# Kernel optimization log

Hardware: AMD Instinct MI355X
Metric: run time of the kernel (lower is better)

Reference implementation:

```python
import jax, jax.numpy as jnp
import numpy as np
import math

HID = 128      # hidden_dim == d_inner (expand=1)
NSTATE = 8     # d_state
K = 4          # scan directions
RANK = math.ceil(HID / 16)  # dt_rank = 8
B, H, W = 4, 64, 64


def _ln(x, g, b, eps=1e-5):
    m = jnp.mean(x, -1, keepdims=True)
    v = jnp.mean((x - m) ** 2, -1, keepdims=True)
    return (x - m) * jax.lax.rsqrt(v + eps) * g + b


def _ss2d(x, in_w, conv_w, conv_b, xproj_w, dt_w, dt_b, A_logs, Ds, ln_g, ln_b, out_w):
    # x: [B,H,W,C] -> VMamba SS2D with d_inner=C, 4-direction selective scan
    Bn, Hh, Ww, C = x.shape
    D, L = C, Hh * Ww
    N = A_logs.shape[-1]
    R = dt_w.shape[-1]
    xz = x @ in_w.T                      # [B,H,W,2D]
    xc, z = jnp.split(xz, 2, axis=-1)
    xc = xc.transpose(0, 3, 1, 2)        # [B,D,H,W]
    xc = jax.lax.conv_general_dilated(xc, conv_w, (1, 1), 'SAME', feature_group_count=D)
    xc = jax.nn.silu(xc + conv_b[None, :, None, None])
    x_hw = xc.reshape(Bn, D, L)
    x_wh = xc.transpose(0, 1, 3, 2).reshape(Bn, D, L)
    xs = jnp.stack([x_hw, x_wh, x_hw[..., ::-1], x_wh[..., ::-1]], 1)  # [B,K,D,L]
    x_dbl = jnp.einsum('bkdl,kcd->bkcl', xs, xproj_w)
    dts, Bs, Cs = x_dbl[:, :, :R], x_dbl[:, :, R:R + N], x_dbl[:, :, R + N:]
    dt = jax.nn.softplus(jnp.einsum('bkrl,kdr->bkdl', dts, dt_w) + dt_b[None, :, :, None])
    A = -jnp.exp(A_logs.reshape(K, D, N))  # [K,D,N]

    def step(h, inp):
        x_t, dt_t, B_t, C_t = inp          # [B,K,D],[B,K,D],[B,K,N],[B,K,N]
        h = h * jnp.exp(dt_t[..., None] * A) + dt_t[..., None] * B_t[:, :, None, :] * x_t[..., None]
        return h, jnp.einsum('bkdn,bkn->bkd', h, C_t)

    h0 = jnp.zeros((Bn, K, D, N), x.dtype)
    _, ys = jax.lax.scan(step, h0, (xs.transpose(3, 0, 1, 2), dt.transpose(3, 0, 1, 2),
                                    Bs.transpose(3, 0, 1, 2), Cs.transpose(3, 0, 1, 2)))
    out_y = ys.transpose(1, 2, 3, 0) + Ds.reshape(K, D)[None, :, :, None] * xs  # [B,K,D,L]
    wh_y = out_y[:, 3, :, ::-1].reshape(Bn, D, Ww, Hh).transpose(0, 1, 3, 2).reshape(Bn, D, L)
    invwh_y = out_y[:, 1].reshape(Bn, D, Ww, Hh).transpose(0, 1, 3, 2).reshape(Bn, D, L)
    y = out_y[:, 0] + out_y[:, 2, :, ::-1] + wh_y + invwh_y
    y = _ln(y.transpose(0, 2, 1).reshape(Bn, Hh, Ww, D), ln_g, ln_b)
    return (y * jax.nn.silu(z)) @ out_w.T


def _enhance(x, g, b, w, bias):
    return jax.nn.gelu(_ln(x, g, b) @ w.T + bias, approximate=False)


def setup_inputs() -> dict:
    key = jax.random.key(0)
    ks = jax.random.split(key, 12)
    f = lambda k, s, sc=0.02: jax.random.normal(k, s, jnp.float32) * sc
    return dict(
        sar_feat=jax.random.normal(ks[0], (B, H, W, HID), jnp.float32),
        opt_feat=jax.random.normal(ks[1], (B, H, W, HID), jnp.float32),
        ss_in_w=f(ks[2], (2, 2 * HID, HID)),
        ss_conv_w=f(ks[3], (2, HID, 1, 3, 3), 0.1),
        ss_conv_b=f(ks[4], (2, HID)),
        ss_xproj_w=f(ks[5], (2, K, RANK + 2 * NSTATE, HID)),
        ss_dt_w=f(ks[6], (2, K, HID, RANK), 0.1),
        ss_dt_b=f(ks[7], (2, K, HID), 0.1),
        ss_Alogs=jnp.tile(jnp.log(jnp.arange(1, NSTATE + 1, dtype=jnp.float32)), (2, K * HID, 1)),
        ss_Ds=jnp.ones((2, K * HID), jnp.float32),
        ss_ln_g=jnp.ones((2, HID), jnp.float32),
        ss_ln_b=jnp.zeros((2, HID), jnp.float32),
        ss_out_w=f(ks[8], (2, HID, HID)),
        enh_ln_g=jnp.ones((2, HID), jnp.float32),
        enh_ln_b=jnp.zeros((2, HID), jnp.float32),
        enh_w=f(ks[9], (2, HID, HID)),
        enh_b=jnp.zeros((2, HID), jnp.float32),
    )


def reference(sar_feat, opt_feat, ss_in_w, ss_conv_w, ss_conv_b, ss_xproj_w, ss_dt_w,
              ss_dt_b, ss_Alogs, ss_Ds, ss_ln_g, ss_ln_b, ss_out_w,
              enh_ln_g, enh_ln_b, enh_w, enh_b):
    # cat([opt,sar],-1)[...,:C] == opt ; cat([sar,opt],-1)[...,:C] == sar (faithful identity slice)
    # index 0 = cross_ss2d_s2o (input opt), index 1 = cross_ss2d_o2s (input sar)
    xin = jnp.stack([opt_feat, sar_feat])
    guided = jax.vmap(_ss2d)(xin, ss_in_w, ss_conv_w, ss_conv_b, ss_xproj_w, ss_dt_w,
                             ss_dt_b, ss_Alogs, ss_Ds, ss_ln_g, ss_ln_b, ss_out_w)
    # enhance params: index 0 = enhance_sar (on sar_guided=guided[1]), index 1 = enhance_opt (on opt_guided=guided[0])
    enh_in = jnp.stack([guided[1], guided[0]])
    enhanced = jax.vmap(_enhance)(enh_in, enh_ln_g, enh_ln_b, enh_w, enh_b)
    return (sar_feat + enhanced[0], opt_feat + enhanced[1])
```

## Files before the change

kernel.cpp:

```cpp
#include <hip/hip_runtime.h>
#include <hip/hip_bf16.h>
#include <math.h>

#define DEV __device__ __forceinline__

static constexpr int LL = 4096;
static constexpr int DD = 128;
static constexpr int SEG = 128;
static constexpr float LOG2E = 1.4426950408889634f;
static constexpr float LN2 = 0.6931471805599453f;

DEV float silu_(float x) { return x / (1.f + __expf(-x)); }
DEV float erf_(float x) {
  const float ax = fabsf(x);
  const float t = 1.f / fmaf(0.3275911f, ax, 1.f);
  float p = fmaf(1.061405429f, t, -1.453152027f);
  p = fmaf(p, t, 1.421413741f);
  p = fmaf(p, t, -0.284496736f);
  p = fmaf(p, t, 0.254829592f);
  p = p * t;
  const float r = 1.f - p * __expf(-ax * ax);
  return x < 0.f ? -r : r;
}
DEV float gelu_(float x) { return 0.5f * x * (1.f + erf_(x * 0.7071067811865475f)); }
DEV float sp_(float x) {
  const float t = __builtin_amdgcn_exp2f(-fabsf(x) * LOG2E);
  return fmaxf(x, 0.f) + LN2 * __builtin_amdgcn_logf(1.f + t);
}

template <int CTRL>
DEV float dpp_add_(float x) {
  int y = __builtin_amdgcn_update_dpp(0, __float_as_int(x), CTRL, 0xF, 0xF, true);
  return x + __int_as_float(y);
}

DEV void seg_base_step(int k, int s, int& base, int& step) {
  if (k == 0)      { base = s * 64;        step = 1;   }
  else if (k == 1) { base = s;             step = 64;  }
  else if (k == 2) { base = 4095 - s * 64; step = -1;  }
  else             { base = 4095 - s;      step = -64; }
}

__global__ __launch_bounds__(256) void k_inproj(
    const float* __restrict__ sar, const float* __restrict__ opt,
    const float* __restrict__ in_w, float* __restrict__ xz) {
  const int lt = blockIdx.x, ct = blockIdx.y, mb = blockIdx.z;
  const int m = mb >> 2;
  const float* __restrict__ x = (m == 0 ? opt : sar) + (size_t)(mb & 3) * (LL * DD);
  const float* __restrict__ W = in_w + (size_t)m * 256 * DD;
  __shared__ float sA[64][68];
  __shared__ float sW[64][68];
  const int tid = threadIdx.x;
  const int tc = tid & 15, tl = tid >> 4;
  float acc[4][4] = {};
  for (int db = 0; db < 2; ++db) {
    __syncthreads();
    for (int idx = tid; idx < 64 * 16; idx += 256) {
      const int r = idx >> 4, d4 = (idx & 15) << 2;
      *(float4*)&sA[r][d4] = *(const float4*)&x[(size_t)(lt * 64 + r) * DD + db * 64 + d4];
      *(float4*)&sW[r][d4] = *(const float4*)&W[(size_t)(ct * 64 + r) * DD + db * 64 + d4];
    }
    __syncthreads();
#pragma unroll 4
    for (int d = 0; d < 64; d += 4) {
      float4 a[4], w[4];
#pragma unroll
      for (int q = 0; q < 4; ++q) a[q] = *(const float4*)&sA[tl * 4 + q][d];
#pragma unroll
      for (int j = 0; j < 4; ++j) w[j] = *(const float4*)&sW[tc + 16 * j][d];
#pragma unroll
      for (int j = 0; j < 4; ++j)
#pragma unroll
        for (int q = 0; q < 4; ++q)
          acc[j][q] += a[q].x * w[j].x + a[q].y * w[j].y + a[q].z * w[j].z + a[q].w * w[j].w;
    }
  }
  float* __restrict__ dst = xz + ((size_t)mb * 256 + ct * 64) * LL + lt * 64;
#pragma unroll
  for (int j = 0; j < 4; ++j) {
    float4 v = make_float4(acc[j][0], acc[j][1], acc[j][2], acc[j][3]);
    *(float4*)&dst[(size_t)(tc + 16 * j) * LL + tl * 4] = v;
  }
}

__global__ __launch_bounds__(256) void k_conv(
    const float* __restrict__ xz, const float* __restrict__ conv_w,
    const float* __restrict__ conv_b, float* __restrict__ xc) {
  const int ht = blockIdx.x, dg = blockIdx.y, mb = blockIdx.z;
  const int m = mb >> 2;
  __shared__ float sIn[8][18][66];
  __shared__ float sOut[1024][8];
  const float* __restrict__ src = xz + ((size_t)mb * 256 + dg * 8) * LL;
  const int tid = threadIdx.x;
  for (int idx = tid; idx < 8 * 18 * 66; idx += 256) {
    const int dd = idx / (18 * 66);
    const int rem = idx - dd * (18 * 66);
    const int hh = rem / 66, ww = rem - hh * 66;
    const int h = ht * 16 + hh - 1, w = ww - 1;
    float v = 0.f;
    if (h >= 0 && h < 64 && w >= 0 && w < 64) v = src[(size_t)dd * LL + h * 64 + w];
    sIn[dd][hh][ww] = v;
  }
  __syncthreads();
  const int dd = tid & 7, wv = tid >> 3;
  const int dch = dg * 8 + dd;
  float wk[9];
#pragma unroll
  for (int t = 0; t < 9; ++t) wk[t] = conv_w[((size_t)m * DD + dch) * 9 + t];
  const float bias = conv_b[m * DD + dch];
  for (int hh = 0; hh < 16; ++hh) {
#pragma unroll
    for (int wh = 0; wh < 2; ++wh) {
      const int w = wv + wh * 32;
      float s = bias;
#pragma unroll
      for (int kh = 0; kh < 3; ++kh)
#pragma unroll
        for (int kw = 0; kw < 3; ++kw)
          s = fmaf(sIn[dd][hh + kh][w + kw], wk[kh * 3 + kw], s);
      sOut[hh * 64 + w][dd] = silu_(s);
    }
  }
  __syncthreads();
  float* __restrict__ dst = xc + (size_t)mb * LL * DD + dg * 8;
#pragma unroll
  for (int r = 0; r < 4; ++r) {
    const int pos = tid + r * 256;
    const int l = ht * 1024 + pos;
    *(float4*)&dst[(size_t)l * DD + 0] = *(const float4*)&sOut[pos][0];
    *(float4*)&dst[(size_t)l * DD + 4] = *(const float4*)&sOut[pos][4];
  }
}

__global__ __launch_bounds__(256) void k_xproj(
    const float* __restrict__ xc, const float* __restrict__ xproj_w,
    float* __restrict__ xdbl) {
  const int lt = blockIdx.x, k = blockIdx.y, mb = blockIdx.z;
  const int m = mb >> 2, mbk = mb * 4 + k;
  __shared__ float sX[64][132];
  __shared__ float sW[24][132];
  const int tid = threadIdx.x;
  const float* __restrict__ src = xc + (size_t)mb * LL * DD;
  int base, step;
  seg_base_step(k, lt, base, step);
  for (int idx = tid; idx < 64 * 32; idx += 256) {
    const int l = idx >> 5, d4 = (idx & 31) << 2;
    *(float4*)&sX[l][d4] = *(const float4*)&src[(size_t)(base + l * step) * DD + d4];
  }
  const float* __restrict__ Wsrc = xproj_w + ((size_t)m * 4 + k) * 24 * DD;
  for (int idx = tid; idx < 24 * 32; idx += 256) {
    const int r = idx >> 5, d4 = (idx & 31) << 2;
    *(float4*)&sW[r][d4] = *(const float4*)&Wsrc[(size_t)r * DD + d4];
  }
  __syncthreads();
  const int l = tid >> 2, cg = tid & 3;
  float acc[6] = {};
#pragma unroll 8
  for (int d = 0; d < 128; d += 4) {
    const float4 xv = *(const float4*)&sX[l][d];
#pragma unroll
    for (int j = 0; j < 6; ++j) {
      const float4 wv = *(const float4*)&sW[cg * 6 + j][d];
      acc[j] += xv.x * wv.x + xv.y * wv.y + xv.z * wv.z + xv.w * wv.w;
    }
  }
  float* __restrict__ dst = xdbl + ((size_t)mbk * LL + lt * 64 + l) * 24 + cg * 6;
#pragma unroll
  for (int j = 0; j < 6; ++j) dst[j] = acc[j];
}


DEV void load_aln2(const float* __restrict__ Alogs, int m, int k, int d,
                   float* __restrict__ aln2, bool& fastp) {
  const float4 a0 = *(const float4*)&Alogs[((size_t)m * 512 + k * DD + d) * 8];
  const float4 a1 = *(const float4*)&Alogs[((size_t)m * 512 + k * DD + d) * 8 + 4];
  aln2[0] = -__expf(a0.x) * LOG2E; aln2[1] = -__expf(a0.y) * LOG2E;
  aln2[2] = -__expf(a0.z) * LOG2E; aln2[3] = -__expf(a0.w) * LOG2E;
  aln2[4] = -__expf(a1.x) * LOG2E; aln2[5] = -__expf(a1.y) * LOG2E;
  aln2[6] = -__expf(a1.z) * LOG2E; aln2[7] = -__expf(a1.w) * LOG2E;
  fastp = true;
#pragma unroll
  for (int n = 1; n < 8; ++n)
    fastp = fastp && (fabsf(aln2[n] - (float)(n + 1) * aln2[0]) <=
                      1e-4f * fabsf(aln2[n]) + 1e-12f);
}

DEV void load_w8(const float* __restrict__ dt_w, int mbk, int d,
                 float* __restrict__ wreg) {
  const float4 w0 = *(const float4*)&dt_w[((size_t)mbk * DD + d) * 8];
  const float4 w1 = *(const float4*)&dt_w[((size_t)mbk * DD + d) * 8 + 4];
  wreg[0] = w0.x; wreg[1] = w0.y; wreg[2] = w0.z; wreg[3] = w0.w;
  wreg[4] = w1.x; wreg[5] = w1.y; wreg[6] = w1.z; wreg[7] = w1.w;
}

template <bool FAST>
DEV void qpow_(float dt, const float* __restrict__ aln2, float* __restrict__ q) {
  if constexpr (FAST) {
    q[0] = __builtin_amdgcn_exp2f(dt * aln2[0]);
    q[1] = q[0] * q[0]; q[2] = q[1] * q[0]; q[3] = q[1] * q[1];
    q[4] = q[3] * q[0]; q[5] = q[3] * q[1]; q[6] = q[3] * q[2]; q[7] = q[3] * q[3];
  } else {
#pragma unroll
    for (int n = 0; n < 8; ++n) q[n] = __builtin_amdgcn_exp2f(dt * aln2[n]);
  }
}

DEV float dt_of_(const float* __restrict__ slds, int j,
                 const float* __restrict__ w, float bw) {
  const float4 t0 = *(const float4*)&slds[j * 24 + 0];
  const float4 t1 = *(const float4*)&slds[j * 24 + 4];
  float s = bw;
  s = fmaf(t0.x, w[0], s); s = fmaf(t0.y, w[1], s);
  s = fmaf(t0.z, w[2], s); s = fmaf(t0.w, w[3], s);
  s = fmaf(t1.x, w[4], s); s = fmaf(t1.y, w[5], s);
  s = fmaf(t1.z, w[6], s); s = fmaf(t1.w, w[7], s);
  return sp_(s);
}

template <bool FAST>
DEV void hstep_(const float* __restrict__ slds, int j, float dt, float x,
                const float* __restrict__ aln2, float* __restrict__ h) {
  const float u = dt * x;
  float q[8];
  qpow_<FAST>(dt, aln2, q);
  const float4 b0 = *(const float4*)&slds[j * 24 + 8];
  const float4 b1 = *(const float4*)&slds[j * 24 + 12];
  h[0] = fmaf(h[0], q[0], u * b0.x);
  h[1] = fmaf(h[1], q[1], u * b0.y);
  h[2] = fmaf(h[2], q[2], u * b0.z);
  h[3] = fmaf(h[3], q[3], u * b0.w);
  h[4] = fmaf(h[4], q[4], u * b1.x);
  h[5] = fmaf(h[5], q[5], u * b1.y);
  h[6] = fmaf(h[6], q[6], u * b1.z);
  h[7] = fmaf(h[7], q[7], u * b1.w);
}

template <bool FAST>
DEV float ystep_(const float* __restrict__ slds, int j, float dt, float x,
                 const float* __restrict__ aln2, float dsv,
                 float* __restrict__ h) {
  const float u = dt * x;
  float q[8];
  qpow_<FAST>(dt, aln2, q);
  const float4 b0 = *(const float4*)&slds[j * 24 + 8];
  const float4 b1 = *(const float4*)&slds[j * 24 + 12];
  const float4 c0 = *(const float4*)&slds[j * 24 + 16];
  const float4 c1 = *(const float4*)&slds[j * 24 + 20];
  float y = dsv * x;
  h[0] = fmaf(h[0], q[0], u * b0.x); y = fmaf(h[0], c0.x, y);
  h[1] = fmaf(h[1], q[1], u * b0.y); y = fmaf(h[1], c0.y, y);
  h[2] = fmaf(h[2], q[2], u * b0.z); y = fmaf(h[2], c0.z, y);
  h[3] = fmaf(h[3], q[3], u * b0.w); y = fmaf(h[3], c0.w, y);
  h[4] = fmaf(h[4], q[4], u * b1.x); y = fmaf(h[4], c1.x, y);
  h[5] = fmaf(h[5], q[5], u * b1.y); y = fmaf(h[5], c1.y, y);
  h[6] = fmaf(h[6], q[6], u * b1.z); y = fmaf(h[6], c1.z, y);
  h[7] = fmaf(h[7], q[7], u * b1.w); y = fmaf(h[7], c1.w, y);
  return y;
}

template <bool FAST>
DEV void loop1d_(const float* __restrict__ sldsA, const float* __restrict__ sldsB,
                 const float* __restrict__ sx, int d,
                 const float* __restrict__ aln2A, const float* __restrict__ aln2B,
                 const float* __restrict__ wA, const float* __restrict__ wB,
                 float bwA, float bwB, float* __restrict__ hA,
                 float* __restrict__ hB, float& dtsA, float& dtsB) {
#pragma unroll 8
  for (int j = 0; j < 32; ++j) {
    const float xA = sx[j * 128 + d];
    const float xB = sx[(31 - j) * 128 + d];
    const float dtA = dt_of_(sldsA, j, wA, bwA);
    const float dtB = dt_of_(sldsB, j, wB, bwB);
    dtsA += dtA; dtsB += dtB;
    hstep_<FAST>(sldsA, j, dtA, xA, aln2A, hA);
    hstep_<FAST>(sldsB, j, dtB, xB, aln2B, hB);
  }
}

__global__ __launch_bounds__(128) void k_scan1(
    const float* __restrict__ xc, const float* __restrict__ xdbl,
    const float* __restrict__ dt_w, const float* __restrict__ dt_b,
    const float* __restrict__ Alogs, float* __restrict__ hend,
    float* __restrict__ Pseg) {
  const int s = blockIdx.x, p = blockIdx.y, mb = blockIdx.z;
  const int m = mb >> 2;
  const int kA = p, kB = p + 2;
  const int sA = s, sB = 127 - s;
  const int mbkA = mb * 4 + kA, mbkB = mb * 4 + kB;
  const int d = threadIdx.x;
  __shared__ float sldsA[32 * 24], sldsB[32 * 24];
  __shared__ float sx[32 * 128];

  const float4* tA = (const float4*)(xdbl + ((size_t)mbkA * LL + sA * 32) * 24);
  const float4* tB = (const float4*)(xdbl + ((size_t)mbkB * LL + sB * 32) * 24);
  ((float4*)sldsA)[d] = tA[d];
  if (d < 64) ((float4*)sldsA)[128 + d] = tA[128 + d];
  ((float4*)sldsB)[d] = tB[d];
  if (d < 64) ((float4*)sldsB)[128 + d] = tB[128 + d];

  const int base0 = (p == 0) ? s * 32 : ((s & 1) * 32) * 64 + (s >> 1);
  const int stepPos = (p == 0) ? 1 : 64;
  const float* __restrict__ xsrc = xc + (size_t)mb * LL * DD;
#pragma unroll
  for (int t = 0; t < 8; ++t) {
    const int idx = d + t * 128;
    const int r = idx >> 5, c4 = (idx & 31) << 2;
    ((float4*)sx)[idx] = *(const float4*)&xsrc[(size_t)(base0 + r * stepPos) * DD + c4];
  }

  float aln2A[8], aln2B[8]; bool fA, fB;
  load_aln2(Alogs, m, kA, d, aln2A, fA);
  load_aln2(Alogs, m, kB, d, aln2B, fB);
  float wA[8], wB[8];
  load_w8(dt_w, mbkA, d, wA);
  load_w8(dt_w, mbkB, d, wB);
  const float bwA = dt_b[(size_t)mbkA * DD + d];
  const float bwB = dt_b[(size_t)mbkB * DD + d];
  __syncthreads();

  float hA[8] = {0, 0, 0, 0, 0, 0, 0, 0};
  float hB[8] = {0, 0, 0, 0, 0, 0, 0, 0};
  float dtsA = 0.f, dtsB = 0.f;
  if (fA && fB)
    loop1d_<true>(sldsA, sldsB, sx, d, aln2A, aln2B, wA, wB, bwA, bwB, hA, hB, dtsA, dtsB);
  else
    loop1d_<false>(sldsA, sldsB, sx, d, aln2A, aln2B, wA, wB, bwA, bwB, hA, hB, dtsA, dtsB);

  {
    float* __restrict__ he = hend + (((size_t)mbkA * SEG + sA) << 10) + d * 8;
    float* __restrict__ pe = Pseg + (((size_t)mbkA * SEG + sA) << 10) + d * 8;
    *(float4*)&he[0] = make_float4(hA[0], hA[1], hA[2], hA[3]);
    *(float4*)&he[4] = make_float4(hA[4], hA[5], hA[6], hA[7]);
    *(float4*)&pe[0] = make_float4(
        __builtin_amdgcn_exp2f(aln2A[0] * dtsA), __builtin_amdgcn_exp2f(aln2A[1] * dtsA),
        __builtin_amdgcn_exp2f(aln2A[2] * dtsA), __builtin_amdgcn_exp2f(aln2A[3] * dtsA));
    *(float4*)&pe[4] = make_float4(
        __builtin_amdgcn_exp2f(aln2A[4] * dtsA), __builtin_amdgcn_exp2f(aln2A[5] * dtsA),
        __builtin_amdgcn_exp2f(aln2A[6] * dtsA), __builtin_amdgcn_exp2f(aln2A[7] * dtsA));
  }
  {
    float* __restrict__ he = hend + (((size_t)mbkB * SEG + sB) << 10) + d * 8;
    float* __restrict__ pe = Pseg + (((size_t)mbkB * SEG + sB) << 10) + d * 8;
    *(float4*)&he[0] = make_float4(hB[0], hB[1], hB[2], hB[3]);
    *(float4*)&he[4] = make_float4(hB[4], hB[5], hB[6], hB[7]);
    *(float4*)&pe[0] = make_float4(
        __builtin_amdgcn_exp2f(aln2B[0] * dtsB), __builtin_amdgcn_exp2f(aln2B[1] * dtsB),
        __builtin_amdgcn_exp2f(aln2B[2] * dtsB), __builtin_amdgcn_exp2f(aln2B[3] * dtsB));
    *(float4*)&pe[4] = make_float4(
        __builtin_amdgcn_exp2f(aln2B[4] * dtsB), __builtin_amdgcn_exp2f(aln2B[5] * dtsB),
        __builtin_amdgcn_exp2f(aln2B[6] * dtsB), __builtin_amdgcn_exp2f(aln2B[7] * dtsB));
  }
}

__global__ __launch_bounds__(256) void k_scan2(
    const float* __restrict__ hend, const float* __restrict__ Pseg,
    float* __restrict__ hin) {
  const int gid = blockIdx.x * 256 + threadIdx.x;
  const int mbk = gid >> 10, dn = gid & 1023;
  const float* __restrict__ P = Pseg + ((size_t)mbk * SEG << 10) + dn;
  const float* __restrict__ E = hend + ((size_t)mbk * SEG << 10) + dn;
  float* __restrict__ O = hin + ((size_t)mbk * SEG << 10) + dn;
  float h = 0.f;
#pragma unroll
  for (int s = 0; s < SEG; ++s) {
    O[(size_t)s << 10] = h;
    if (s < SEG - 1) h = fmaf(P[(size_t)s << 10], h, E[(size_t)s << 10]);
  }
}

template <bool FAST>
DEV void loop3d_(const float* __restrict__ sldsA, const float* __restrict__ sldsB,
                 const float* __restrict__ sx, int d,
                 const float* __restrict__ aln2A, const float* __restrict__ aln2B,
                 const float* __restrict__ wA, const float* __restrict__ wB,
                 float bwA, float bwB, float dsvA, float dsvB,
                 float* __restrict__ hA, float* __restrict__ hB,
                 float* __restrict__ yA, float* __restrict__ yB,
                 ptrdiff_t sstep) {
#pragma unroll 8
  for (int j = 0; j < 32; ++j) {
    const float xA = sx[j * 128 + d];
    const float xB = sx[(31 - j) * 128 + d];
    const float dtA = dt_of_(sldsA, j, wA, bwA);
    const float dtB = dt_of_(sldsB, j, wB, bwB);
    const float vA = ystep_<FAST>(sldsA, j, dtA, xA, aln2A, dsvA, hA);
    const float vB = ystep_<FAST>(sldsB, j, dtB, xB, aln2B, dsvB, hB);
    yA[(ptrdiff_t)j * sstep] = vA;
    yB[(ptrdiff_t)(31 - j) * sstep] = vB;
  }
}

__global__ __launch_bounds__(128) void k_scan3(
    const float* __restrict__ xc, const float* __restrict__ xdbl,
    const float* __restrict__ dt_w, const float* __restrict__ dt_b,
    const float* __restrict__ Alogs, const float* __restrict__ Ds,
    const float* __restrict__ hin, float* __restrict__ y0,
    float* __restrict__ y1, float* __restrict__ y2, float* __restrict__ y3) {
  const int s = blockIdx.x, p = blockIdx.y, mb = blockIdx.z;
  const int m = mb >> 2;
  const int kA = p, kB = p + 2;
  const int sA = s, sB = 127 - s;
  const int mbkA = mb * 4 + kA, mbkB = mb * 4 + kB;
  const int d = threadIdx.x;
  __shared__ float sldsA[32 * 24], sldsB[32 * 24];
  __shared__ float sx[32 * 128];

  const float4* tA = (const float4*)(xdbl + ((size_t)mbkA * LL + sA * 32) * 24);
  const float4* tB = (const float4*)(xdbl + ((size_t)mbkB * LL + sB * 32) * 24);
  ((float4*)sldsA)[d] = tA[d];
  if (d < 64) ((float4*)sldsA)[128 + d] = tA[128 + d];
  ((float4*)sldsB)[d] = tB[d];
  if (d < 64) ((float4*)sldsB)[128 + d] = tB[128 + d];

  const int base0 = (p == 0) ? s * 32 : ((s & 1) * 32) * 64 + (s >> 1);
  const int stepPos = (p == 0) ? 1 : 64;
  const float* __restrict__ xsrc = xc + (size_t)mb * LL * DD;
#pragma unroll
  for (int t = 0; t < 8; ++t) {
    const int idx = d + t * 128;
    const int r = idx >> 5, c4 = (idx & 31) << 2;
    ((float4*)sx)[idx] = *(const float4*)&xsrc[(size_t)(base0 + r * stepPos) * DD + c4];
  }

  float aln2A[8], aln2B[8]; bool fA, fB;
  load_aln2(Alogs, m, kA, d, aln2A, fA);
  load_aln2(Alogs, m, kB, d, aln2B, fB);
  float wA[8], wB[8];
  load_w8(dt_w, mbkA, d, wA);
  load_w8(dt_w, mbkB, d, wB);
  const float bwA = dt_b[(size_t)mbkA * DD + d];
  const float bwB = dt_b[(size_t)mbkB * DD + d];
  const float dsvA = Ds[(size_t)m * 512 + kA * DD + d];
  const float dsvB = Ds[(size_t)m * 512 + kB * DD + d];

  float hA[8], hB[8];
  {
    const float* hp = hin + (((size_t)mbkA * SEG + sA) << 10) + d * 8;
    const float4 h0 = *(const float4*)&hp[0];
    const float4 h1 = *(const float4*)&hp[4];
    hA[0] = h0.x; hA[1] = h0.y; hA[2] = h0.z; hA[3] = h0.w;
    hA[4] = h1.x; hA[5] = h1.y; hA[6] = h1.z; hA[7] = h1.w;
  }
  {
    const float* hp = hin + (((size_t)mbkB * SEG + sB) << 10) + d * 8;
    const float4 h0 = *(const float4*)&hp[0];
    const float4 h1 = *(const float4*)&hp[4];
    hB[0] = h0.x; hB[1] = h0.y; hB[2] = h0.z; hB[3] = h0.w;
    hB[4] = h1.x; hB[5] = h1.y; hB[6] = h1.z; hB[7] = h1.w;
  }

  const size_t off0 = (size_t)mb * LL * DD + (size_t)base0 * DD + d;
  float* __restrict__ yA = (p == 0 ? y0 : y1) + off0;
  float* __restrict__ yB = (p == 0 ? y2 : y3) + off0;
  const ptrdiff_t sstep = (ptrdiff_t)stepPos * DD;
  __syncthreads();

  if (fA && fB)
    loop3d_<true>(sldsA, sldsB, sx, d, aln2A, aln2B, wA, wB, bwA, bwB,
                  dsvA, dsvB, hA, hB, yA, yB, sstep);
  else
    loop3d_<false>(sldsA, sldsB, sx, d, aln2A, aln2B, wA, wB, bwA, bwB,
                   dsvA, dsvB, hA, hB, yA, yB, sstep);
}

__global__ __launch_bounds__(256) void k_outproj(
    const float* __restrict__ y0, const float* __restrict__ y1,
    const float* __restrict__ y2, const float* __restrict__ y3,
    const float* __restrict__ xz, const float* __restrict__ ln_g,
    const float* __restrict__ ln_b, const float* __restrict__ out_w,
    float* __restrict__ guided) {
  const int lt = blockIdx.x, mb = blockIdx.y;
  const int m = mb >> 2;
  __shared__ float sv[32][132];
  __shared__ float sW[64][68];
  __shared__ float smr[32][2];
  __shared__ float sg[128], sb[128];
  const int tid = threadIdx.x;
  const size_t yoff = ((size_t)mb * LL + lt * 32) * DD;
  const float4* p0 = (const float4*)(y0 + yoff);
  const float4* p1 = (const float4*)(y1 + yoff);
  const float4* p2 = (const float4*)(y2 + yoff);
  const float4* p3 = (const float4*)(y3 + yoff);
  float4 ya[4], yb[4], yc4[4], yd4[4];
#pragma unroll
  for (int t = 0; t < 4; ++t) {
    ya[t] = p0[tid + t * 256]; yb[t] = p1[tid + t * 256];
    yc4[t] = p2[tid + t * 256]; yd4[t] = p3[tid + t * 256];
  }
  const int zc = tid >> 1, zh = tid & 1;
  const float4* zsrc = (const float4*)(xz + ((size_t)mb * 256 + 128 + zc) * LL + lt * 32 + zh * 16);
  float4 zv[4];
#pragma unroll
  for (int t = 0; t < 4; ++t) zv[t] = zsrc[t];
  const float* __restrict__ Wp = out_w + (size_t)m * DD * DD;
  float4 wpre[4];
#pragma unroll
  for (int t = 0; t < 4; ++t) {
    const int idx = tid + t * 256;
    wpre[t] = *(const float4*)&Wp[(size_t)(idx >> 4) * DD + ((idx & 15) << 2)];
  }
  if (tid < 128) { sg[tid] = ln_g[m * DD + tid]; sb[tid] = ln_b[m * DD + tid]; }
#pragma unroll
  for (int t = 0; t < 4; ++t) {
    const int idx = tid + t * 256;
    float4 v;
    v.x = (ya[t].x + yb[t].x) + (yc4[t].x + yd4[t].x);
    v.y = (ya[t].y + yb[t].y) + (yc4[t].y + yd4[t].y);
    v.z = (ya[t].z + yb[t].z) + (yc4[t].z + yd4[t].z);
    v.w = (ya[t].w + yb[t].w) + (yc4[t].w + yd4[t].w);
    *(float4*)&sv[idx >> 5][(idx & 31) << 2] = v;
  }
  __syncthreads();
  {
    const int l = tid >> 3, q = tid & 7;
    float s = 0.f, s2 = 0.f;
#pragma unroll
    for (int d0 = 0; d0 < 16; d0 += 4) {
      const float4 v = *(const float4*)&sv[l][q * 16 + d0];
      s += v.x + v.y + v.z + v.w;
      s2 += v.x * v.x + v.y * v.y + v.z * v.z + v.w * v.w;
    }
    s = dpp_add_<0xB1>(s); s = dpp_add_<0x4E>(s); s = dpp_add_<0x141>(s);
    s2 = dpp_add_<0xB1>(s2); s2 = dpp_add_<0x4E>(s2); s2 = dpp_add_<0x141>(s2);
    if (q == 0) {
      const float mean = s * (1.f / 128.f);
      smr[l][0] = mean;
      smr[l][1] = rsqrtf(fmaf(s2, 1.f / 128.f, -mean * mean) + 1e-5f);
    }
  }
  __syncthreads();
  {
    const float g = sg[zc], bb = sb[zc];
    const float* zf = (const float*)zv;
#pragma unroll
    for (int i2 = 0; i2 < 16; ++i2) {
      const int l = zh * 16 + i2;
      const float v = fmaf((sv[l][zc] - smr[l][0]) * smr[l][1], g, bb);
      sv[l][zc] = v * silu_(zf[i2]);
    }
  }
  const int tc = tid & 15, tl = tid >> 4;
  float* __restrict__ dst = guided + ((size_t)mb * LL + lt * 32) * DD;
#pragma unroll
  for (int jb = 0; jb < 2; ++jb) {
    float acc[4][2] = {};
#pragma unroll
    for (int db = 0; db < 2; ++db) {
      __syncthreads();
#pragma unroll
      for (int t = 0; t < 4; ++t) {
        const int idx = tid + t * 256;
        *(float4*)&sW[idx >> 4][(idx & 15) << 2] = wpre[t];
      }
      const int ph = jb * 2 + db + 1;
      if (ph < 4) {
        const int jb2 = ph >> 1, db2 = ph & 1;
#pragma unroll
        for (int t = 0; t < 4; ++t) {
          const int idx = tid + t * 256;
          wpre[t] = *(const float4*)&Wp[(size_t)(jb2 * 64 + (idx >> 4)) * DD + db2 * 64 + ((idx & 15) << 2)];
        }
      }
      __syncthreads();
#pragma unroll 4
      for (int d0 = 0; d0 < 64; d0 += 4) {
        float4 av[2], wv[4];
#pragma unroll
        for (int q = 0; q < 2; ++q) av[q] = *(const float4*)&sv[tl * 2 + q][db * 64 + d0];
#pragma unroll
        for (int j = 0; j < 4; ++j) wv[j] = *(const float4*)&sW[tc + 16 * j][d0];
#pragma unroll
        for (int j = 0; j < 4; ++j)
#pragma unroll
          for (int q = 0; q < 2; ++q)
            acc[j][q] += av[q].x * wv[j].x + av[q].y * wv[j].y + av[q].z * wv[j].z + av[q].w * wv[j].w;
      }
    }
#pragma unroll
    for (int j = 0; j < 4; ++j)
#pragma unroll
      for (int q = 0; q < 2; ++q)
        dst[(size_t)(tl * 2 + q) * DD + jb * 64 + tc + 16 * j] = acc[j][q];
  }
}

__global__ __launch_bounds__(256) void k_enhance(
    const float* __restrict__ guided, const float* __restrict__ eg,
    const float* __restrict__ ebv, const float* __restrict__ ew,
    const float* __restrict__ ebias, const float* __restrict__ sar,
    const float* __restrict__ opt, float* __restrict__ outp) {
  const int lt = blockIdx.x, ib = blockIdx.y;
  const int i = ib >> 2, b = ib & 3;
  __shared__ float sv[32][132];
  __shared__ float sW[64][68];
  __shared__ float smr[32][2];
  __shared__ float sg[128], sb2[128], sbias[128];
  const int tid = threadIdx.x;
  const float4* gsrc =
      (const float4*)(guided + (((size_t)(1 - i) * 4 + b) * LL + lt * 32) * DD);
  float4 gv[4];
#pragma unroll
  for (int t = 0; t < 4; ++t) gv[t] = gsrc[tid + t * 256];
  const float* __restrict__ Wp = ew + (size_t)i * DD * DD;
  float4 wpre[4];
#pragma unroll
  for (int t = 0; t < 4; ++t) {
    const int idx = tid + t * 256;
    wpre[t] = *(const float4*)&Wp[(size_t)(idx >> 4) * DD + ((idx & 15) << 2)];
  }
  if (tid < 128) {
    sg[tid] = eg[i * DD + tid];
    sb2[tid] = ebv[i * DD + tid];
    sbias[tid] = ebias[i * DD + tid];
  }
#pragma unroll
  for (int t = 0; t < 4; ++t) {
    const int idx = tid + t * 256;
    *(float4*)&sv[idx >> 5][(idx & 31) << 2] = gv[t];
  }
  __syncthreads();
  {
    const int l = tid >> 3, q = tid & 7;
    float s = 0.f, s2 = 0.f;
#pragma unroll
    for (int d0 = 0; d0 < 16; d0 += 4) {
      const float4 v = *(const float4*)&sv[l][q * 16 + d0];
      s += v.x + v.y + v.z + v.w;
      s2 += v.x * v.x + v.y * v.y + v.z * v.z + v.w * v.w;
    }
    s = dpp_add_<0xB1>(s); s = dpp_add_<0x4E>(s); s = dpp_add_<0x141>(s);
    s2 = dpp_add_<0xB1>(s2); s2 = dpp_add_<0x4E>(s2); s2 = dpp_add_<0x141>(s2);
    if (q == 0) {
      const float mean = s * (1.f / 128.f);
      smr[l][0] = mean;
      smr[l][1] = rsqrtf(fmaf(s2, 1.f / 128.f, -mean * mean) + 1e-5f);
    }
  }
  __syncthreads();
  {
    const int c = tid >> 1, half = tid & 1;
    const float g = sg[c], bb = sb2[c];
#pragma unroll
    for (int i2 = 0; i2 < 16; ++i2) {
      const int l = half * 16 + i2;
      sv[l][c] = fmaf((sv[l][c] - smr[l][0]) * smr[l][1], g, bb);
    }
  }
  const int tc = tid & 15, tl = tid >> 4;
  const float* __restrict__ resid = (i == 0 ? sar : opt) + ((size_t)b * LL + lt * 32) * DD;
  float* __restrict__ dst = outp + (size_t)i * (4 * LL * DD) + ((size_t)b * LL + lt * 32) * DD;
  float rv[16];
#pragma unroll
  for (int jb = 0; jb < 2; ++jb)
#pragma unroll
    for (int j = 0; j < 4; ++j)
#pragma unroll
      for (int q = 0; q < 2; ++q)
        rv[jb * 8 + j * 2 + q] = resid[(size_t)(tl * 2 + q) * DD + jb * 64 + tc + 16 * j];
  float accA[4][2] = {}, accB[4][2] = {};
#pragma unroll
  for (int jb = 0; jb < 2; ++jb) {
#pragma unroll
    for (int db = 0; db < 2; ++db) {
      __syncthreads();
#pragma unroll
      for (int t = 0; t < 4; ++t) {
        const int idx = tid + t * 256;
        *(float4*)&sW[idx >> 4][(idx & 15) << 2] = wpre[t];
      }
      const int ph = jb * 2 + db + 1;
      if (ph < 4) {
        const int jb2 = ph >> 1, db2 = ph & 1;
#pragma unroll
        for (int t = 0; t < 4; ++t) {
          const int idx = tid + t * 256;
          wpre[t] = *(const float4*)&Wp[(size_t)(jb2 * 64 + (idx >> 4)) * DD + db2 * 64 + ((idx & 15) << 2)];
        }
      }
      __syncthreads();
      float (*acc)[2] = (jb == 0) ? accA : accB;
#pragma unroll 4
      for (int d0 = 0; d0 < 64; d0 += 4) {
        float4 av[2], wv[4];
#pragma unroll
        for (int q = 0; q < 2; ++q) av[q] = *(const float4*)&sv[tl * 2 + q][db * 64 + d0];
#pragma unroll
        for (int j = 0; j < 4; ++j) wv[j] = *(const float4*)&sW[tc + 16 * j][d0];
#pragma unroll
        for (int j = 0; j < 4; ++j)
#pragma unroll
          for (int q = 0; q < 2; ++q)
            acc[j][q] += av[q].x * wv[j].x + av[q].y * wv[j].y + av[q].z * wv[j].z + av[q].w * wv[j].w;
      }
    }
  }
#pragma unroll
  for (int jb = 0; jb < 2; ++jb)
#pragma unroll
    for (int j = 0; j < 4; ++j)
#pragma unroll
      for (int q = 0; q < 2; ++q) {
        const int col = jb * 64 + tc + 16 * j;
        const float u = ((jb == 0) ? accA[j][q] : accB[j][q]) + sbias[col];
        dst[(size_t)(tl * 2 + q) * DD + col] = rv[jb * 8 + j * 2 + q] + gelu_(u);
      }
}

extern "C" void kernel_launch(void* const* d_in, const int* in_sizes, int n_in,
                              void* d_out, int out_size, void* d_ws, size_t ws_size,
                              hipStream_t stream) {
  (void)in_sizes; (void)n_in; (void)out_size; (void)ws_size;
  const float* sar    = (const float*)d_in[0];
  const float* opt    = (const float*)d_in[1];
  const float* in_w   = (const float*)d_in[2];
  const float* conv_w = (const float*)d_in[3];
  const float* conv_b = (const float*)d_in[4];
  const float* xproj_w= (const float*)d_in[5];
  const float* dt_w   = (const float*)d_in[6];
  const float* dt_b   = (const float*)d_in[7];
  const float* Alogs  = (const float*)d_in[8];
  const float* Ds     = (const float*)d_in[9];
  const float* ln_g   = (const float*)d_in[10];
  const float* ln_b   = (const float*)d_in[11];
  const float* out_w  = (const float*)d_in[12];
  const float* eg     = (const float*)d_in[13];
  const float* eb     = (const float*)d_in[14];
  const float* ew     = (const float*)d_in[15];
  const float* ebias  = (const float*)d_in[16];

  float* ws     = (float*)d_ws;
  float* xz     = ws;
  float* xc     = xz + 8388608;
  float* xdbl   = xc + 4194304;
  float* y0b    = xdbl + 3145728;
  float* y1b    = y0b + 4194304;
  float* y2b    = y1b + 4194304;
  float* y3b    = y2b + 4194304;
  float* guided = y3b + 4194304;
  float* hend   = guided + 4194304;
  float* Pseg   = hend + 4194304;
  float* hin    = Pseg + 4194304;
  float* outf   = (float*)d_out;

  k_inproj <<<dim3(64, 4, 8), 256, 0, stream>>>(sar, opt, in_w, xz);
  k_conv   <<<dim3(4, 16, 8), 256, 0, stream>>>(xz, conv_w, conv_b, xc);
  k_xproj  <<<dim3(64, 4, 8), 256, 0, stream>>>(xc, xproj_w, xdbl);
  k_scan1  <<<dim3(128, 2, 8), 128, 0, stream>>>(xc, xdbl, dt_w, dt_b, Alogs, hend, Pseg);
  k_scan2  <<<dim3(128), 256, 0, stream>>>(hend, Pseg, hin);
  k_scan3  <<<dim3(128, 2, 8), 128, 0, stream>>>(xc, xdbl, dt_w, dt_b, Alogs, Ds, hin,
                                                 y0b, y1b, y2b, y3b);
  k_outproj<<<dim3(128, 8), 256, 0, stream>>>(y0b, y1b, y2b, y3b, xz, ln_g, ln_b, out_w, guided);
  k_enhance<<<dim3(128, 8), 256, 0, stream>>>(guided, eg, eb, ew, ebias, sar, opt, outf);
}
```

Baseline: 265.4 us.

## Merge forward/reverse scan outputs in-register, read xdbl directly, batch scan2 loads

In k_scan3 the forward and reversed direction chains are now run one after the other per thread. The forward results are kept in a 32-entry register array and added to the reverse chain's outputs before writing. This halves the y buffers from four to two and cuts k_outproj's reads to match. Both scan kernels drop their shared-memory staging of xdbl and read it straight from global memory through cached, thread-uniform loads. k_scan2 now batches its P/E loads 16 at a time to expose memory parallelism. The cost is higher register pressure, and the A and B chains no longer interleave for ILP.

```diff
diff --git a/kernel.cpp b/kernel.cpp
--- a/kernel.cpp
+++ b/kernel.cpp
@@ -205,10 +205,10 @@
   }
 }
 
-DEV float dt_of_(const float* __restrict__ slds, int j,
+DEV float dt_of_(const float* __restrict__ t24,
                  const float* __restrict__ w, float bw) {
-  const float4 t0 = *(const float4*)&slds[j * 24 + 0];
-  const float4 t1 = *(const float4*)&slds[j * 24 + 4];
+  const float4 t0 = *(const float4*)&t24[0];
+  const float4 t1 = *(const float4*)&t24[4];
   float s = bw;
   s = fmaf(t0.x, w[0], s); s = fmaf(t0.y, w[1], s);
   s = fmaf(t0.z, w[2], s); s = fmaf(t0.w, w[3], s);
@@ -218,13 +218,13 @@
 }
 
 template <bool FAST>
-DEV void hstep_(const float* __restrict__ slds, int j, float dt, float x,
+DEV void hstep_(const float* __restrict__ t24, float dt, float x,
                 const float* __restrict__ aln2, float* __restrict__ h) {
   const float u = dt * x;
   float q[8];
   qpow_<FAST>(dt, aln2, q);
-  const float4 b0 = *(const float4*)&slds[j * 24 + 8];
-  const float4 b1 = *(const float4*)&slds[j * 24 + 12];
+  const float4 b0 = *(const float4*)&t24[8];
+  const float4 b1 = *(const float4*)&t24[12];
   h[0] = fmaf(h[0], q[0], u * b0.x);
   h[1] = fmaf(h[1], q[1], u * b0.y);
   h[2] = fmaf(h[2], q[2], u * b0.z);
@@ -236,16 +236,16 @@
 }
 
 template <bool FAST>
-DEV float ystep_(const float* __restrict__ slds, int j, float dt, float x,
+DEV float ystep_(const float* __restrict__ t24, float dt, float x,
                  const float* __restrict__ aln2, float dsv,
                  float* __restrict__ h) {
   const float u = dt * x;
   float q[8];
   qpow_<FAST>(dt, aln2, q);
-  const float4 b0 = *(const float4*)&slds[j * 24 + 8];
-  const float4 b1 = *(const float4*)&slds[j * 24 + 12];
-  const float4 c0 = *(const float4*)&slds[j * 24 + 16];
-  const float4 c1 = *(const float4*)&slds[j * 24 + 20];
+  const float4 b0 = *(const float4*)&t24[8];
+  const float4 b1 = *(const float4*)&t24[12];
+  const float4 c0 = *(const float4*)&t24[16];
+  const float4 c1 = *(const float4*)&t24[20];
   float y = dsv * x;
   h[0] = fmaf(h[0], q[0], u * b0.x); y = fmaf(h[0], c0.x, y);
   h[1] = fmaf(h[1], q[1], u * b0.y); y = fmaf(h[1], c0.y, y);
@@ -259,7 +259,7 @@
 }
 
 template <bool FAST>
-DEV void loop1d_(const float* __restrict__ sldsA, const float* __restrict__ sldsB,
+DEV void loop1d_(const float* __restrict__ tA, const float* __restrict__ tB,
                  const float* __restrict__ sx, int d,
                  const float* __restrict__ aln2A, const float* __restrict__ aln2B,
                  const float* __restrict__ wA, const float* __restrict__ wB,
@@ -269,11 +269,11 @@
   for (int j = 0; j < 32; ++j) {
     const float xA = sx[j * 128 + d];
     const float xB = sx[(31 - j) * 128 + d];
-    const float dtA = dt_of_(sldsA, j, wA, bwA);
-    const float dtB = dt_of_(sldsB, j, wB, bwB);
+    const float dtA = dt_of_(tA + j * 24, wA, bwA);
+    const float dtB = dt_of_(tB + j * 24, wB, bwB);
     dtsA += dtA; dtsB += dtB;
-    hstep_<FAST>(sldsA, j, dtA, xA, aln2A, hA);
-    hstep_<FAST>(sldsB, j, dtB, xB, aln2B, hB);
+    hstep_<FAST>(tA + j * 24, dtA, xA, aln2A, hA);
+    hstep_<FAST>(tB + j * 24, dtB, xB, aln2B, hB);
   }
 }
 
@@ -288,15 +288,10 @@
   const int sA = s, sB = 127 - s;
   const int mbkA = mb * 4 + kA, mbkB = mb * 4 + kB;
   const int d = threadIdx.x;
-  __shared__ float sldsA[32 * 24], sldsB[32 * 24];
   __shared__ float sx[32 * 128];
 
-  const float4* tA = (const float4*)(xdbl + ((size_t)mbkA * LL + sA * 32) * 24);
-  const float4* tB = (const float4*)(xdbl + ((size_t)mbkB * LL + sB * 32) * 24);
-  ((float4*)sldsA)[d] = tA[d];
-  if (d < 64) ((float4*)sldsA)[128 + d] = tA[128 + d];
-  ((float4*)sldsB)[d] = tB[d];
-  if (d < 64) ((float4*)sldsB)[128 + d] = tB[128 + d];
+  const float* __restrict__ tA = xdbl + ((size_t)mbkA * LL + sA * 32) * 24;
+  const float* __restrict__ tB = xdbl + ((size_t)mbkB * LL + sB * 32) * 24;
 
   const int base0 = (p == 0) ? s * 32 : ((s & 1) * 32) * 64 + (s >> 1);
   const int stepPos = (p == 0) ? 1 : 64;
@@ -322,9 +317,9 @@
   float hB[8] = {0, 0, 0, 0, 0, 0, 0, 0};
   float dtsA = 0.f, dtsB = 0.f;
   if (fA && fB)
-    loop1d_<true>(sldsA, sldsB, sx, d, aln2A, aln2B, wA, wB, bwA, bwB, hA, hB, dtsA, dtsB);
+    loop1d_<true>(tA, tB, sx, d, aln2A, aln2B, wA, wB, bwA, bwB, hA, hB, dtsA, dtsB);
   else
-    loop1d_<false>(sldsA, sldsB, sx, d, aln2A, aln2B, wA, wB, bwA, bwB, hA, hB, dtsA, dtsB);
+    loop1d_<false>(tA, tB, sx, d, aln2A, aln2B, wA, wB, bwA, bwB, hA, hB, dtsA, dtsB);
 
   {
     float* __restrict__ he = hend + (((size_t)mbkA * SEG + sA) << 10) + d * 8;
@@ -361,32 +356,47 @@
   const float* __restrict__ E = hend + ((size_t)mbk * SEG << 10) + dn;
   float* __restrict__ O = hin + ((size_t)mbk * SEG << 10) + dn;
   float h = 0.f;
-#pragma unroll
-  for (int s = 0; s < SEG; ++s) {
-    O[(size_t)s << 10] = h;
-    if (s < SEG - 1) h = fmaf(P[(size_t)s << 10], h, E[(size_t)s << 10]);
+  for (int c0 = 0; c0 < SEG; c0 += 16) {
+    float pv[16], ev[16];
+#pragma unroll
+    for (int t = 0; t < 16; ++t) {
+      pv[t] = P[(size_t)(c0 + t) << 10];
+      ev[t] = E[(size_t)(c0 + t) << 10];
+    }
+#pragma unroll
+    for (int t = 0; t < 16; ++t) {
+      O[(size_t)(c0 + t) << 10] = h;
+      h = fmaf(pv[t], h, ev[t]);
+    }
   }
 }
 
 template <bool FAST>
-DEV void loop3d_(const float* __restrict__ sldsA, const float* __restrict__ sldsB,
-                 const float* __restrict__ sx, int d,
-                 const float* __restrict__ aln2A, const float* __restrict__ aln2B,
-                 const float* __restrict__ wA, const float* __restrict__ wB,
-                 float bwA, float bwB, float dsvA, float dsvB,
-                 float* __restrict__ hA, float* __restrict__ hB,
-                 float* __restrict__ yA, float* __restrict__ yB,
+DEV void chainA_(const float* __restrict__ t24, const float* __restrict__ sx, int d,
+                 const float* __restrict__ aln2, const float* __restrict__ w,
+                 float bw, float dsv, float* __restrict__ h,
+                 float* __restrict__ va) {
+#pragma unroll
+  for (int j = 0; j < 32; ++j) {
+    const float x = sx[j * 128 + d];
+    const float dt = dt_of_(t24 + j * 24, w, bw);
+    va[j] = ystep_<FAST>(t24 + j * 24, dt, x, aln2, dsv, h);
+  }
+}
+
+template <bool FAST>
+DEV void chainB_(const float* __restrict__ t24, const float* __restrict__ sx, int d,
+                 const float* __restrict__ aln2, const float* __restrict__ w,
+                 float bw, float dsv, float* __restrict__ h,
+                 const float* __restrict__ va, float* __restrict__ yd,
                  ptrdiff_t sstep) {
-#pragma unroll 8
+#pragma unroll
   for (int j = 0; j < 32; ++j) {
-    const float xA = sx[j * 128 + d];
-    const float xB = sx[(31 - j) * 128 + d];
-    const float dtA = dt_of_(sldsA, j, wA, bwA);
-    const float dtB = dt_of_(sldsB, j, wB, bwB);
-    const float vA = ystep_<FAST>(sldsA, j, dtA, xA, aln2A, dsvA, hA);
-    const float vB = ystep_<FAST>(sldsB, j, dtB, xB, aln2B, dsvB, hB);
-    yA[(ptrdiff_t)j * sstep] = vA;
-    yB[(ptrdiff_t)(31 - j) * sstep] = vB;
+    const int phys = 31 - j;
+    const float x = sx[phys * 128 + d];
+    const float dt = dt_of_(t24 + j * 24, w, bw);
+    const float v = ystep_<FAST>(t24 + j * 24, dt, x, aln2, dsv, h);
+    yd[(ptrdiff_t)phys * sstep] = v + va[phys];
   }
 }
 
@@ -394,23 +404,18 @@
     const float* __restrict__ xc, const float* __restrict__ xdbl,
     const float* __restrict__ dt_w, const float* __restrict__ dt_b,
     const float* __restrict__ Alogs, const float* __restrict__ Ds,
-    const float* __restrict__ hin, float* __restrict__ y0,
-    float* __restrict__ y1, float* __restrict__ y2, float* __restrict__ y3) {
+    const float* __restrict__ hin, float* __restrict__ yrow,
+    float* __restrict__ ycol) {
   const int s = blockIdx.x, p = blockIdx.y, mb = blockIdx.z;
   const int m = mb >> 2;
   const int kA = p, kB = p + 2;
   const int sA = s, sB = 127 - s;
   const int mbkA = mb * 4 + kA, mbkB = mb * 4 + kB;
   const int d = threadIdx.x;
-  __shared__ float sldsA[32 * 24], sldsB[32 * 24];
   __shared__ float sx[32 * 128];
 
-  const float4* tA = (const float4*)(xdbl + ((size_t)mbkA * LL + sA * 32) * 24);
-  const float4* tB = (const float4*)(xdbl + ((size_t)mbkB * LL + sB * 32) * 24);
-  ((float4*)sldsA)[d] = tA[d];
-  if (d < 64) ((float4*)sldsA)[128 + d] = tA[128 + d];
-  ((float4*)sldsB)[d] = tB[d];
-  if (d < 64) ((float4*)sldsB)[128 + d] = tB[128 + d];
+  const float* __restrict__ tA = xdbl + ((size_t)mbkA * LL + sA * 32) * 24;
+  const float* __restrict__ tB = xdbl + ((size_t)mbkB * LL + sB * 32) * 24;
 
   const int base0 = (p == 0) ? s * 32 : ((s & 1) * 32) * 64 + (s >> 1);
   const int stepPos = (p == 0) ? 1 : 64;
@@ -450,22 +455,19 @@
   }
 
   const size_t off0 = (size_t)mb * LL * DD + (size_t)base0 * DD + d;
-  float* __restrict__ yA = (p == 0 ? y0 : y1) + off0;
-  float* __restrict__ yB = (p == 0 ? y2 : y3) + off0;
+  float* __restrict__ yd = (p == 0 ? yrow : ycol) + off0;
   const ptrdiff_t sstep = (ptrdiff_t)stepPos * DD;
   __syncthreads();
 
-  if (fA && fB)
-    loop3d_<true>(sldsA, sldsB, sx, d, aln2A, aln2B, wA, wB, bwA, bwB,
-                  dsvA, dsvB, hA, hB, yA, yB, sstep);
-  else
-    loop3d_<false>(sldsA, sldsB, sx, d, aln2A, aln2B, wA, wB, bwA, bwB,
-                   dsvA, dsvB, hA, hB, yA, yB, sstep);
+  float va[32];
+  if (fA) chainA_<true>(tA, sx, d, aln2A, wA, bwA, dsvA, hA, va);
+  else    chainA_<false>(tA, sx, d, aln2A, wA, bwA, dsvA, hA, va);
+  if (fB) chainB_<true>(tB, sx, d, aln2B, wB, bwB, dsvB, hB, va, yd, sstep);
+  else    chainB_<false>(tB, sx, d, aln2B, wB, bwB, dsvB, hB, va, yd, sstep);
 }
 
 __global__ __launch_bounds__(256) void k_outproj(
-    const float* __restrict__ y0, const float* __restrict__ y1,
-    const float* __restrict__ y2, const float* __restrict__ y3,
+    const float* __restrict__ yrow, const float* __restrict__ ycol,
     const float* __restrict__ xz, const float* __restrict__ ln_g,
     const float* __restrict__ ln_b, const float* __restrict__ out_w,
     float* __restrict__ guided) {
@@ -477,16 +479,11 @@
   __shared__ float sg[128], sb[128];
   const int tid = threadIdx.x;
   const size_t yoff = ((size_t)mb * LL + lt * 32) * DD;
-  const float4* p0 = (const float4*)(y0 + yoff);
-  const float4* p1 = (const float4*)(y1 + yoff);
-  const float4* p2 = (const float4*)(y2 + yoff);
-  const float4* p3 = (const float4*)(y3 + yoff);
-  float4 ya[4], yb[4], yc4[4], yd4[4];
-#pragma unroll
-  for (int t = 0; t < 4; ++t) {
-    ya[t] = p0[tid + t * 256]; yb[t] = p1[tid + t * 256];
-    yc4[t] = p2[tid + t * 256]; yd4[t] = p3[tid + t * 256];
-  }
+  const float4* p0 = (const float4*)(yrow + yoff);
+  const float4* p1 = (const float4*)(ycol + yoff);
+  float4 ya[4], yb[4];
+#pragma unroll
+  for (int t = 0; t < 4; ++t) { ya[t] = p0[tid + t * 256]; yb[t] = p1[tid + t * 256]; }
   const int zc = tid >> 1, zh = tid & 1;
   const float4* zsrc = (const float4*)(xz + ((size_t)mb * 256 + 128 + zc) * LL + lt * 32 + zh * 16);
   float4 zv[4];
@@ -504,10 +501,8 @@
   for (int t = 0; t < 4; ++t) {
     const int idx = tid + t * 256;
     float4 v;
-    v.x = (ya[t].x + yb[t].x) + (yc4[t].x + yd4[t].x);
-    v.y = (ya[t].y + yb[t].y) + (yc4[t].y + yd4[t].y);
-    v.z = (ya[t].z + yb[t].z) + (yc4[t].z + yd4[t].z);
-    v.w = (ya[t].w + yb[t].w) + (yc4[t].w + yd4[t].w);
+    v.x = ya[t].x + yb[t].x; v.y = ya[t].y + yb[t].y;
+    v.z = ya[t].z + yb[t].z; v.w = ya[t].w + yb[t].w;
     *(float4*)&sv[idx >> 5][(idx & 31) << 2] = v;
   }
   __syncthreads();
@@ -732,11 +727,9 @@
   float* xz     = ws;
   float* xc     = xz + 8388608;
   float* xdbl   = xc + 4194304;
-  float* y0b    = xdbl + 3145728;
-  float* y1b    = y0b + 4194304;
-  float* y2b    = y1b + 4194304;
-  float* y3b    = y2b + 4194304;
-  float* guided = y3b + 4194304;
+  float* yrowb  = xdbl + 3145728;
+  float* ycolb  = yrowb + 4194304;
+  float* guided = ycolb + 4194304;
   float* hend   = guided + 4194304;
   float* Pseg   = hend + 4194304;
   float* hin    = Pseg + 4194304;
@@ -748,7 +741,7 @@
   k_scan1  <<<dim3(128, 2, 8), 128, 0, stream>>>(xc, xdbl, dt_w, dt_b, Alogs, hend, Pseg);
   k_scan2  <<<dim3(128), 256, 0, stream>>>(hend, Pseg, hin);
   k_scan3  <<<dim3(128, 2, 8), 128, 0, stream>>>(xc, xdbl, dt_w, dt_b, Alogs, Ds, hin,
-                                                 y0b, y1b, y2b, y3b);
-  k_outproj<<<dim3(128, 8), 256, 0, stream>>>(y0b, y1b, y2b, y3b, xz, ln_g, ln_b, out_w, guided);
+                                                 yrowb, ycolb);
+  k_outproj<<<dim3(128, 8), 256, 0, stream>>>(yrowb, ycolb, xz, ln_g, ln_b, out_w, guided);
   k_enhance<<<dim3(128, 8), 256, 0, stream>>>(guided, eg, eb, ew, ebias, sar, opt, outf);
 }
```

After: 265.4 us. Within noise of the previous version (-0.0%).
